# Performance work log

Hardware: AMD Instinct MI355X
Metric: run time of the kernel (lower is better)

The kernel has to match this reference:

```python
import jax, jax.numpy as jnp
import numpy as np

N = 100000      # nodes
E = 800000      # directed edges (self-loops added in reference, PyG default)
F_IN = 16
H1, C1 = 3, 32  # conv1: heads=3, out=32 (concat -> 96)
H2, C2 = 1, 32  # conv2: heads=1, out=32
NC = 16         # n_channel
SLOPE = 0.2     # PyG GATConv default negative_slope


def setup_inputs() -> dict:
    key = jax.random.key(0)
    ks = jax.random.split(key, 12)
    s = 0.1
    return {
        "x": jax.random.normal(ks[0], (N, F_IN), jnp.float32),
        "edge_index": jax.random.randint(ks[1], (2, E), 0, N, dtype=jnp.int32),
        "W1": jax.random.normal(ks[2], (F_IN, H1 * C1), jnp.float32) * s,
        "a_src1": jax.random.normal(ks[3], (H1, C1), jnp.float32) * s,
        "a_dst1": jax.random.normal(ks[4], (H1, C1), jnp.float32) * s,
        "b1": jnp.zeros((H1 * C1,), jnp.float32),
        "W2": jax.random.normal(ks[5], (H1 * C1, H2 * C2), jnp.float32) * s,
        "a_src2": jax.random.normal(ks[6], (H2, C2), jnp.float32) * s,
        "a_dst2": jax.random.normal(ks[7], (H2, C2), jnp.float32) * s,
        "b2": jnp.zeros((H2 * C2,), jnp.float32),
        "Wf": jax.random.normal(ks[8], (C2, NC), jnp.float32) * s,
        "bf": jnp.zeros((NC,), jnp.float32),
    }


def _gat_layer(x, src, dst, W, a_s, a_d, b, heads, outc):
    # x: [N, Fin]; src/dst: [Etot]
    h = (x @ W).reshape(N, heads, outc)                        # [N, H, C]
    alpha_s = (h * a_s).sum(-1)                                # [N, H]
    alpha_d = (h * a_d).sum(-1)                                # [N, H]
    e = jax.nn.leaky_relu(alpha_s[src] + alpha_d[dst], SLOPE)  # [Etot, H]
    # scatter-softmax over edges grouped by destination node
    m = jax.ops.segment_max(e, dst, num_segments=N)            # [N, H]
    p = jnp.exp(e - m[dst])
    z = jax.ops.segment_sum(p, dst, num_segments=N)
    alpha = p / (z[dst] + 1e-16)                               # [Etot, H]
    out = jax.ops.segment_sum(h[src] * alpha[:, :, None], dst, num_segments=N)
    return out.reshape(N, heads * outc) + b


def reference(x, edge_index, W1, a_src1, a_dst1, b1, W2, a_src2, a_dst2, b2, Wf, bf):
    loops = jnp.arange(N, dtype=edge_index.dtype)  # PyG add_self_loops=True
    src = jnp.concatenate([edge_index[0], loops])
    dst = jnp.concatenate([edge_index[1], loops])
    h = jax.nn.selu(_gat_layer(x, src, dst, W1, a_src1, a_dst1, b1, H1, C1))
    h = jax.nn.selu(_gat_layer(h, src, dst, W2, a_src2, a_dst2, b2, H2, C2))
    return h @ Wf + bf
```

## Files before the change

### kernel.cpp

```cpp
#include <hip/hip_runtime.h>
#include <hip/hip_bf16.h>

#define N_NODES 100000
#define N_EDGES 800000
#define F_IN    16
#define H1      3
#define C1      32
#define F1      (H1*C1)
#define F2      32
#define NC      16
#define SLOPE       0.2f
#define SELU_SCALE  1.0507009873554805f
#define SELU_ALPHA  1.6732632423543772f

#define DEG_PAD 48

#define NSLICE        8
#define BLK_PER_SLICE 256
#define SCAT_BLKS     (NSLICE * BLK_PER_SLICE)
#define EDGES_PER_BLK (N_EDGES / BLK_PER_SLICE)
#define SLICE_NODES   (N_NODES / NSLICE)
#define XB_NB   ((N_NODES + 255) / 256)

typedef unsigned short ushort_t;

__device__ __forceinline__ ushort_t f2bf(float f) {
    unsigned u = __float_as_uint(f);
    return (ushort_t)((u + 0x7FFFu + ((u >> 16) & 1u)) >> 16);
}
__device__ __forceinline__ unsigned pack2bf(float a, float b) {
    return (unsigned)f2bf(a) | ((unsigned)f2bf(b) << 16);
}
__device__ __forceinline__ float bf_lo(unsigned u) { return __uint_as_float(u << 16); }
__device__ __forceinline__ float bf_hi(unsigned u) { return __uint_as_float(u & 0xFFFF0000u); }

__device__ __forceinline__ void unpack8(const uint4 v, float* f) {
    f[0] = bf_lo(v.x); f[1] = bf_hi(v.x);
    f[2] = bf_lo(v.y); f[3] = bf_hi(v.y);
    f[4] = bf_lo(v.z); f[5] = bf_hi(v.z);
    f[6] = bf_lo(v.w); f[7] = bf_hi(v.w);
}
__device__ __forceinline__ float selu_f(float u) {
    return u > 0.f ? SELU_SCALE * u : SELU_SCALE * SELU_ALPHA * (__expf(u) - 1.f);
}

__global__ __launch_bounds__(256) void build_k(
    const int* __restrict__ ei, const float* __restrict__ x,
    const float* __restrict__ W1, const float* __restrict__ aS1,
    const float* __restrict__ aD1,
    int* __restrict__ deg, int* __restrict__ colp,
    uint4* __restrict__ xb, float4* __restrict__ as4, float4* __restrict__ ad4)
{
    __shared__ float swv[F_IN * 6];
    const int b = blockIdx.x, t = threadIdx.x;
    if (b < SCAT_BLKS) {
        const int slice = b & 7;
        const int lo = slice * SLICE_NODES, hi = lo + SLICE_NODES;
        const int e0 = (b >> 3) * EDGES_PER_BLK;
        int* cslice = colp + (size_t)slice * DEG_PAD * SLICE_NODES;
        for (int e = e0 + t; e < e0 + EDGES_PER_BLK; e += 256) {
            const int d = __builtin_nontemporal_load(ei + N_EDGES + e);
            if (d >= lo && d < hi) {
                const int s = __builtin_nontemporal_load(ei + e);
                const int pos = atomicAdd(&deg[d], 1);
                if (pos < DEG_PAD) cslice[pos * SLICE_NODES + (d - lo)] = s;
            }
        }
    } else {
        if (t < 96) {
            const int k = t / 6, j = t % 6;
            const int h = (j < 3) ? j : j - 3;
            const float* a = (j < 3) ? aS1 : aD1;
            float acc = 0.f;
#pragma unroll
            for (int c = 0; c < 32; ++c) acc += W1[k * F1 + h * 32 + c] * a[h * 32 + c];
            swv[k * 6 + j] = acc;
        }
        __syncthreads();
        const int node = (b - SCAT_BLKS) * 256 + t;
        if (node < N_NODES) {
            float xr[16];
            const float4* xp = reinterpret_cast<const float4*>(&x[(size_t)node * F_IN]);
            const float4 v0 = xp[0], v1 = xp[1], v2 = xp[2], v3 = xp[3];
            xr[0] = v0.x; xr[1] = v0.y; xr[2]  = v0.z; xr[3]  = v0.w;
            xr[4] = v1.x; xr[5] = v1.y; xr[6]  = v1.z; xr[7]  = v1.w;
            xr[8] = v2.x; xr[9] = v2.y; xr[10] = v2.z; xr[11] = v2.w;
            xr[12] = v3.x; xr[13] = v3.y; xr[14] = v3.z; xr[15] = v3.w;
            uint4 o0, o1;
            o0.x = pack2bf(xr[0], xr[1]);   o0.y = pack2bf(xr[2], xr[3]);
            o0.z = pack2bf(xr[4], xr[5]);   o0.w = pack2bf(xr[6], xr[7]);
            o1.x = pack2bf(xr[8], xr[9]);   o1.y = pack2bf(xr[10], xr[11]);
            o1.z = pack2bf(xr[12], xr[13]); o1.w = pack2bf(xr[14], xr[15]);
            xb[(size_t)node * 2]     = o0;
            xb[(size_t)node * 2 + 1] = o1;
            float sacc[3] = {0.f, 0.f, 0.f}, dacc[3] = {0.f, 0.f, 0.f};
#pragma unroll
            for (int k = 0; k < 16; ++k) {
                const float xk = xr[k];
#pragma unroll
                for (int j = 0; j < 3; ++j) {
                    sacc[j] += xk * swv[k * 6 + j];
                    dacc[j] += xk * swv[k * 6 + 3 + j];
                }
            }
            as4[node] = make_float4(sacc[0], sacc[1], sacc[2], 0.f);
            ad4[node] = make_float4(dacc[0], dacc[1], dacc[2], 0.f);
        }
    }
}

__global__ __launch_bounds__(256) void agg1_k(
    const int* __restrict__ deg, const int* __restrict__ colp,
    const uint4* __restrict__ xb,
    const float4* __restrict__ as4, const float4* __restrict__ ad4,
    uint4* __restrict__ xagg_b)
{
    const int t = threadIdx.x;
    const int node = blockIdx.x * 64 + (t >> 2);
    const int u = t & 1;
    const int v = (t >> 1) & 1;
    if (node >= N_NODES) return;
    const int slice = node / SLICE_NODES;
    const int dl = node - slice * SLICE_NODES;
    const int* cbase = colp + (size_t)slice * DEG_PAD * SLICE_NODES + dl;
    const int dg = min(deg[node], DEG_PAD);
    const float4 adv = ad4[node];

    float acc[3][8];
#pragma unroll
    for (int h = 0; h < 3; ++h)
#pragma unroll
        for (int i = 0; i < 8; ++i) acc[h][i] = 0.f;
    float z0 = 0.f, z1 = 0.f, z2 = 0.f;
    if (v == 0) {
        const float4 a = as4[node];
        float e0 = a.x + adv.x; e0 = e0 > 0.f ? e0 : SLOPE * e0;
        float e1 = a.y + adv.y; e1 = e1 > 0.f ? e1 : SLOPE * e1;
        float e2 = a.z + adv.z; e2 = e2 > 0.f ? e2 : SLOPE * e2;
        const float p0 = __expf(e0), p1 = __expf(e1), p2 = __expf(e2);
        z0 = p0; z1 = p1; z2 = p2;
        float xf[8]; unpack8(xb[(size_t)node * 2 + u], xf);
#pragma unroll
        for (int i = 0; i < 8; ++i) {
            acc[0][i] = p0 * xf[i]; acc[1][i] = p1 * xf[i]; acc[2][i] = p2 * xf[i];
        }
    }
    int j = v; uint4 hv; float4 av;
    if (j < dg) { const int s = cbase[j * SLICE_NODES]; av = as4[s]; hv = xb[(size_t)s * 2 + u]; }
    while (j < dg) {
        const uint4 cx = hv; const float4 ca = av;
        const int jn = j + 2;
        if (jn < dg) {
            const int s = cbase[jn * SLICE_NODES];
            av = as4[s]; hv = xb[(size_t)s * 2 + u];
        }
        float e0 = ca.x + adv.x; e0 = e0 > 0.f ? e0 : SLOPE * e0;
        float e1 = ca.y + adv.y; e1 = e1 > 0.f ? e1 : SLOPE * e1;
        float e2 = ca.z + adv.z; e2 = e2 > 0.f ? e2 : SLOPE * e2;
        const float p0 = __expf(e0), p1 = __expf(e1), p2 = __expf(e2);
        z0 += p0; z1 += p1; z2 += p2;
        float xf[8]; unpack8(cx, xf);
#pragma unroll
        for (int i = 0; i < 8; ++i) {
            acc[0][i] += p0 * xf[i]; acc[1][i] += p1 * xf[i]; acc[2][i] += p2 * xf[i];
        }
        j = jn;
    }
    z0 += __shfl_xor(z0, 2); z1 += __shfl_xor(z1, 2); z2 += __shfl_xor(z2, 2);
#pragma unroll
    for (int h = 0; h < 3; ++h)
#pragma unroll
        for (int i = 0; i < 8; ++i) acc[h][i] += __shfl_xor(acc[h][i], 2);
    if (v == 0) {
        const float zi[3] = {1.f / (z0 + 1e-16f), 1.f / (z1 + 1e-16f), 1.f / (z2 + 1e-16f)};
#pragma unroll
        for (int h = 0; h < 3; ++h) {
            uint4 o;
            o.x = pack2bf(acc[h][0] * zi[h], acc[h][1] * zi[h]);
            o.y = pack2bf(acc[h][2] * zi[h], acc[h][3] * zi[h]);
            o.z = pack2bf(acc[h][4] * zi[h], acc[h][5] * zi[h]);
            o.w = pack2bf(acc[h][6] * zi[h], acc[h][7] * zi[h]);
            xagg_b[(size_t)node * 6 + h * 2 + u] = o;
        }
    }
}

__global__ __launch_bounds__(384) void l12_k(
    const uint4* __restrict__ xagg_b, const float* __restrict__ W1,
    const float* __restrict__ b1, const float* __restrict__ W2,
    const float* __restrict__ aS2, const float* __restrict__ aD2,
    ushort_t* __restrict__ h2b, float* __restrict__ as2, float* __restrict__ ad2)
{
    __shared__ float sxa[64 * 48];
    __shared__ float sx2[64][F1 + 1];
    __shared__ float swv[F1 * 2];
    const int t = threadIdx.x;
    const int node0 = blockIdx.x * 64;

    {
        const int nl = t / 6, w = t - nl * 6;
        const int node = node0 + nl;
        uint4 vv = make_uint4(0, 0, 0, 0);
        if (node < N_NODES) vv = xagg_b[(size_t)node * 6 + w];
        float xf[8]; unpack8(vv, xf);
        float* dst = &sxa[nl * 48 + w * 8];
        *reinterpret_cast<float4*>(dst)     = make_float4(xf[0], xf[1], xf[2], xf[3]);
        *reinterpret_cast<float4*>(dst + 4) = make_float4(xf[4], xf[5], xf[6], xf[7]);
    }
    if (t < 192) {
        const int k = t >> 1, j = t & 1;
        const float* a = j ? aD2 : aS2;
        float acc = 0.f;
#pragma unroll
        for (int c = 0; c < 32; ++c) acc += W2[k * F2 + c] * a[c];
        swv[k * 2 + j] = acc;
    }
    __syncthreads();

    {
        const int ng = t / 48;
        const int cp = t - ng * 48;
        const int c0 = cp * 2, c1 = c0 + 1;
        const int hc = c0 >> 5;
        float w0[16], w1[16];
#pragma unroll
        for (int k = 0; k < 16; ++k) { w0[k] = W1[k * F1 + c0]; w1[k] = W1[k * F1 + c1]; }
        const float bc0 = b1[c0], bc1 = b1[c1];
#pragma unroll
        for (int nn = 0; nn < 8; ++nn) {
            const int n = ng * 8 + nn;
            const float4* xp = reinterpret_cast<const float4*>(&sxa[n * 48 + hc * 16]);
            const float4 a0 = xp[0], a1 = xp[1], a2 = xp[2], a3 = xp[3];
            const float xa[16] = {a0.x, a0.y, a0.z, a0.w, a1.x, a1.y, a1.z, a1.w,
                                  a2.x, a2.y, a2.z, a2.w, a3.x, a3.y, a3.z, a3.w};
            float acc0 = bc0, acc1 = bc1;
#pragma unroll
            for (int k = 0; k < 16; ++k) { acc0 += xa[k] * w0[k]; acc1 += xa[k] * w1[k]; }
            sx2[n][c0] = selu_f(acc0);
            sx2[n][c1] = selu_f(acc1);
        }
    }
    __syncthreads();

    if (t < 256) {
        const int cq = t & 7;
        const int np = t >> 3;
        const int n0 = np * 2, n1 = n0 + 1;
        float acc0[4] = {0.f, 0.f, 0.f, 0.f}, acc1[4] = {0.f, 0.f, 0.f, 0.f};
#pragma unroll 4
        for (int k = 0; k < F1; ++k) {
            const float4 w = *reinterpret_cast<const float4*>(&W2[k * F2 + cq * 4]);
            const float x0 = sx2[n0][k], x1 = sx2[n1][k];
            acc0[0] += x0 * w.x; acc0[1] += x0 * w.y; acc0[2] += x0 * w.z; acc0[3] += x0 * w.w;
            acc1[0] += x1 * w.x; acc1[1] += x1 * w.y; acc1[2] += x1 * w.z; acc1[3] += x1 * w.w;
        }
        if (node0 + n0 < N_NODES) {
            uint2 o; o.x = pack2bf(acc0[0], acc0[1]); o.y = pack2bf(acc0[2], acc0[3]);
            *reinterpret_cast<uint2*>(&h2b[(size_t)(node0 + n0) * F2 + cq * 4]) = o;
        }
        if (node0 + n1 < N_NODES) {
            uint2 o; o.x = pack2bf(acc1[0], acc1[1]); o.y = pack2bf(acc1[2], acc1[3]);
            *reinterpret_cast<uint2*>(&h2b[(size_t)(node0 + n1) * F2 + cq * 4]) = o;
        }
        if (cq < 2) {
            float s0 = 0.f, s1 = 0.f;
#pragma unroll 4
            for (int k = 0; k < F1; ++k) {
                const float wv = swv[k * 2 + cq];
                s0 += sx2[n0][k] * wv; s1 += sx2[n1][k] * wv;
            }
            if (cq == 0) {
                if (node0 + n0 < N_NODES) as2[node0 + n0] = s0;
                if (node0 + n1 < N_NODES) as2[node0 + n1] = s1;
            } else {
                if (node0 + n0 < N_NODES) ad2[node0 + n0] = s0;
                if (node0 + n1 < N_NODES) ad2[node0 + n1] = s1;
            }
        }
    }
}

__global__ __launch_bounds__(256) void agg2_final_k(
    const int* __restrict__ deg, const int* __restrict__ colp,
    const ushort_t* __restrict__ hb,
    const float* __restrict__ as, const float* __restrict__ ad,
    const float* __restrict__ b2, const float* __restrict__ Wf,
    const float* __restrict__ bf, float* __restrict__ out)
{
    __shared__ float sW[F2 * NC];
    __shared__ float sx[64][33];
    const int t = threadIdx.x;
    for (int i = t; i < F2 * NC; i += 256) sW[i] = Wf[i];
    const int sub = t >> 2;
    const int u = t & 1;
    const int v = (t >> 1) & 1;
    const int node = blockIdx.x * 64 + sub;
    const bool valid = node < N_NODES;

    if (valid) {
        const int slice = node / SLICE_NODES;
        const int dl = node - slice * SLICE_NODES;
        const int* cbase = colp + (size_t)slice * DEG_PAD * SLICE_NODES + dl;
        const int dg = min(deg[node], DEG_PAD);
        const float adv = ad[node];
        float acc[16];
#pragma unroll
        for (int i = 0; i < 16; ++i) acc[i] = 0.f;
        float z = 0.f;
        if (v == 0) {
            float e = as[node] + adv; e = e > 0.f ? e : SLOPE * e;
            const float pv = __expf(e);
            z = pv;
            const uint4* hp = reinterpret_cast<const uint4*>(&hb[(size_t)node * F2 + u * 16]);
            float xf[8];
            unpack8(hp[0], xf);
#pragma unroll
            for (int i = 0; i < 8; ++i) acc[i] = pv * xf[i];
            unpack8(hp[1], xf);
#pragma unroll
            for (int i = 0; i < 8; ++i) acc[8 + i] = pv * xf[i];
        }
        int j = v; uint4 hva, hvb; float asv;
        if (j < dg) {
            const int s = cbase[j * SLICE_NODES];
            asv = as[s];
            const uint4* hp = reinterpret_cast<const uint4*>(&hb[(size_t)s * F2 + u * 16]);
            hva = hp[0]; hvb = hp[1];
        }
        while (j < dg) {
            const uint4 ca = hva, cb = hvb; const float cas = asv;
            const int jn = j + 2;
            if (jn < dg) {
                const int s = cbase[jn * SLICE_NODES];
                asv = as[s];
                const uint4* hp = reinterpret_cast<const uint4*>(&hb[(size_t)s * F2 + u * 16]);
                hva = hp[0]; hvb = hp[1];
            }
            float e = cas + adv; e = e > 0.f ? e : SLOPE * e;
            const float pv = __expf(e);
            z += pv;
            float xf[8];
            unpack8(ca, xf);
#pragma unroll
            for (int i = 0; i < 8; ++i) acc[i] += pv * xf[i];
            unpack8(cb, xf);
#pragma unroll
            for (int i = 0; i < 8; ++i) acc[8 + i] += pv * xf[i];
            j = jn;
        }
        z += __shfl_xor(z, 2);
#pragma unroll
        for (int i = 0; i < 16; ++i) acc[i] += __shfl_xor(acc[i], 2);
        if (v == 0) {
            const float zi = 1.f / (z + 1e-16f);
#pragma unroll
            for (int i = 0; i < 16; ++i)
                sx[sub][u * 16 + i] = selu_f(acc[i] * zi + b2[u * 16 + i]);
        }
    }
    __syncthreads();
    if (valid) {
        const int c0 = (t & 3) * 4;
        float r[4];
#pragma unroll
        for (int i = 0; i < 4; ++i) r[i] = bf[c0 + i];
#pragma unroll
        for (int k = 0; k < F2; ++k) {
            const float xk = sx[sub][k];
#pragma unroll
            for (int i = 0; i < 4; ++i) r[i] += xk * sW[k * NC + c0 + i];
        }
        *reinterpret_cast<float4*>(&out[(size_t)node * NC + c0]) =
            make_float4(r[0], r[1], r[2], r[3]);
    }
}

extern "C" void kernel_launch(void* const* d_in, const int* in_sizes, int n_in,
                              void* d_out, int out_size, void* d_ws, size_t ws_size,
                              hipStream_t stream)
{
    const float* x    = (const float*)d_in[0];
    const int*   ei   = (const int*)d_in[1];
    const float* W1   = (const float*)d_in[2];
    const float* aS1  = (const float*)d_in[3];
    const float* aD1  = (const float*)d_in[4];
    const float* b1   = (const float*)d_in[5];
    const float* W2   = (const float*)d_in[6];
    const float* aS2  = (const float*)d_in[7];
    const float* aD2  = (const float*)d_in[8];
    const float* b2   = (const float*)d_in[9];
    const float* Wf   = (const float*)d_in[10];
    const float* bf   = (const float*)d_in[11];
    float* out = (float*)d_out;

    uint4*    xb     = (uint4*)d_ws;
    float4*   as4    = (float4*)(xb + (size_t)N_NODES * 2);
    float4*   ad4    = as4 + N_NODES;
    uint4*    xagg_b = (uint4*)(ad4 + N_NODES);
    ushort_t* h2b    = (ushort_t*)(xagg_b + (size_t)N_NODES * 6);
    float*    as2    = (float*)(h2b + (size_t)N_NODES * F2);
    float*    ad2    = as2 + N_NODES;
    int*      colp   = (int*)(ad2 + N_NODES);
    int*      deg    = colp + (size_t)N_NODES * DEG_PAD;

    hipMemsetAsync(deg, 0, sizeof(int) * N_NODES, stream);
    build_k<<<SCAT_BLKS + XB_NB, 256, 0, stream>>>(
        ei, x, W1, aS1, aD1, deg, colp, xb, as4, ad4);
    agg1_k<<<(N_NODES + 63) / 64, 256, 0, stream>>>(deg, colp, xb, as4, ad4, xagg_b);
    l12_k<<<(N_NODES + 63) / 64, 384, 0, stream>>>(
        xagg_b, W1, b1, W2, aS2, aD2, h2b, as2, ad2);
    agg2_final_k<<<(N_NODES + 63) / 64, 256, 0, stream>>>(
        deg, colp, h2b, as2, ad2, b2, Wf, bf, out);
}
```

Measured before the change: 150.9 us.

## Split edge scatter into wave-ballot binning pass and separate CSR scatter kernel

Edge bucketing by destination slice now happens in two kernels. The first compacts matching (src, local dst) pairs into a per-block bin buffer using a wave ballot and one shared atomic per wave. A new second kernel then does the per-node degree atomics and the column writes. This removes the divergent per-lane global atomics and scattered writes from the filtering pass, at the cost of an extra launch and an extra round trip through the bin buffer. Bins are capped at 512 entries and overflowing edges overwrite the last slot, which is only correct if no block exceeds the cap (about 391 expected per block).

Result: no change. 148.7 us (-1.4%).

```diff
diff --git a/kernel.cpp b/kernel.cpp
--- a/kernel.cpp
+++ b/kernel.cpp
@@ -21,6 +21,7 @@
 #define EDGES_PER_BLK (N_EDGES / BLK_PER_SLICE)
 #define SLICE_NODES   (N_NODES / NSLICE)
 #define XB_NB   ((N_NODES + 255) / 256)
+#define BIN_CAP 512
 
 typedef unsigned short ushort_t;
 
@@ -44,28 +45,42 @@
     return u > 0.f ? SELU_SCALE * u : SELU_SCALE * SELU_ALPHA * (__expf(u) - 1.f);
 }
 
-__global__ __launch_bounds__(256) void build_k(
+__global__ __launch_bounds__(256) void bin_k(
     const int* __restrict__ ei, const float* __restrict__ x,
     const float* __restrict__ W1, const float* __restrict__ aS1,
     const float* __restrict__ aD1,
-    int* __restrict__ deg, int* __restrict__ colp,
+    uint2* __restrict__ binbuf, int* __restrict__ gcnt,
     uint4* __restrict__ xb, float4* __restrict__ as4, float4* __restrict__ ad4)
 {
     __shared__ float swv[F_IN * 6];
+    __shared__ int scnt;
     const int b = blockIdx.x, t = threadIdx.x;
     if (b < SCAT_BLKS) {
+        if (t == 0) scnt = 0;
+        __syncthreads();
         const int slice = b & 7;
         const int lo = slice * SLICE_NODES, hi = lo + SLICE_NODES;
         const int e0 = (b >> 3) * EDGES_PER_BLK;
-        int* cslice = colp + (size_t)slice * DEG_PAD * SLICE_NODES;
+        uint2* buf = binbuf + (size_t)b * BIN_CAP;
+        const int lane = t & 63;
         for (int e = e0 + t; e < e0 + EDGES_PER_BLK; e += 256) {
-            const int d = __builtin_nontemporal_load(ei + N_EDGES + e);
-            if (d >= lo && d < hi) {
-                const int s = __builtin_nontemporal_load(ei + e);
-                const int pos = atomicAdd(&deg[d], 1);
-                if (pos < DEG_PAD) cslice[pos * SLICE_NODES + (d - lo)] = s;
+            const int d = ei[N_EDGES + e];
+            const bool pred = (d >= lo) && (d < hi);
+            const unsigned long long mask = __ballot(pred);
+            if (mask) {
+                const int leader = (int)(__ffsll((unsigned long long)mask) - 1);
+                int base = 0;
+                if (lane == leader) base = atomicAdd(&scnt, (int)__popcll(mask));
+                base = __shfl(base, leader);
+                if (pred) {
+                    const int off = (int)__popcll(mask & ((1ull << lane) - 1ull));
+                    const int pos = min(base + off, BIN_CAP - 1);
+                    buf[pos] = make_uint2((unsigned)ei[e], (unsigned)(d - lo));
+                }
             }
         }
+        __syncthreads();
+        if (t == 0) gcnt[b] = min(scnt, BIN_CAP);
     } else {
         if (t < 96) {
             const int k = t / 6, j = t % 6;
@@ -109,6 +124,24 @@
     }
 }
 
+__global__ __launch_bounds__(256) void scat_k(
+    const uint2* __restrict__ binbuf, const int* __restrict__ gcnt,
+    int* __restrict__ deg, int* __restrict__ colp)
+{
+    const int b = blockIdx.x;
+    const int slice = b & 7;
+    const int lo = slice * SLICE_NODES;
+    const int n = gcnt[b];
+    const uint2* buf = binbuf + (size_t)b * BIN_CAP;
+    int* cslice = colp + (size_t)slice * DEG_PAD * SLICE_NODES;
+    for (int i = threadIdx.x; i < n; i += 256) {
+        const uint2 e = buf[i];
+        const int dl = (int)e.y;
+        const int pos = atomicAdd(&deg[lo + dl], 1);
+        if (pos < DEG_PAD) cslice[pos * SLICE_NODES + dl] = (int)e.x;
+    }
+}
+
 __global__ __launch_bounds__(256) void agg1_k(
     const int* __restrict__ deg, const int* __restrict__ colp,
     const uint4* __restrict__ xb,
@@ -402,10 +435,13 @@
     float*    ad2    = as2 + N_NODES;
     int*      colp   = (int*)(ad2 + N_NODES);
     int*      deg    = colp + (size_t)N_NODES * DEG_PAD;
+    uint2*    binbuf = (uint2*)(deg + N_NODES);
+    int*      gcnt   = (int*)(binbuf + (size_t)SCAT_BLKS * BIN_CAP);
 
     hipMemsetAsync(deg, 0, sizeof(int) * N_NODES, stream);
-    build_k<<<SCAT_BLKS + XB_NB, 256, 0, stream>>>(
-        ei, x, W1, aS1, aD1, deg, colp, xb, as4, ad4);
+    bin_k<<<SCAT_BLKS + XB_NB, 256, 0, stream>>>(
+        ei, x, W1, aS1, aD1, binbuf, gcnt, xb, as4, ad4);
+    scat_k<<<SCAT_BLKS, 256, 0, stream>>>(binbuf, gcnt, deg, colp);
     agg1_k<<<(N_NODES + 63) / 64, 256, 0, stream>>>(deg, colp, xb, as4, ad4, xagg_b);
     l12_k<<<(N_NODES + 63) / 64, 384, 0, stream>>>(
         xagg_b, W1, b1, W2, aS2, aD2, h2b, as2, ad2);
```
